# Optimization experiments

Measured on AMD Instinct MI355X. Metric: run time of the kernel, lower is better.

## Reference

```python
import jax, jax.numpy as jnp
import numpy as np
from jax import nn as jnn

N = 100000      # nodes
E = 3200000     # edges (avg degree 32)
G = 1024        # graphs in batch
F_IN = 3        # num_features (hard-coded in module)
D = 32          # dim (hard-coded in module)
BN_EPS = 1e-5


def setup_inputs() -> dict:
    key = jax.random.key(0)
    ks = jax.random.split(key, 24)
    def lin(k, i, o):
        return (jax.random.normal(k, (i, o), jnp.float32) / np.sqrt(i)).astype(jnp.float32)
    inp = {}
    inp["x"] = jax.random.normal(ks[0], (N, F_IN), jnp.float32)
    inp["edge_index"] = jax.random.randint(ks[1], (2, E), 0, N, dtype=jnp.int32)
    inp["batch"] = jnp.sort(jax.random.randint(ks[2], (N,), 0, G, dtype=jnp.int32))
    idx = 3
    in_dims = [F_IN, D, D]
    for l in (1, 2, 3):
        inp[f"W{l}a"] = lin(ks[idx], in_dims[l - 1], D); idx += 1
        inp[f"b{l}a"] = jnp.zeros((D,), jnp.float32)
        inp[f"W{l}b"] = lin(ks[idx], D, D); idx += 1
        inp[f"b{l}b"] = jnp.zeros((D,), jnp.float32)
        inp[f"g{l}"] = jnp.ones((D,), jnp.float32)            # BN gamma
        inp[f"be{l}"] = jnp.zeros((D,), jnp.float32)          # BN beta
        inp[f"m{l}"] = 0.1 * jax.random.normal(ks[idx], (D,), jnp.float32); idx += 1  # running mean
        inp[f"v{l}"] = jax.random.uniform(ks[idx], (D,), jnp.float32, 0.5, 1.5); idx += 1  # running var
    inp["Wf1"] = lin(ks[idx], D, D); idx += 1
    inp["bf1"] = jnp.zeros((D,), jnp.float32)
    inp["Wf2"] = lin(ks[idx], D, 1)
    inp["bf2"] = jnp.zeros((1,), jnp.float32)
    return inp


def reference(x, edge_index, batch,
              W1a, b1a, W1b, b1b, g1, be1, m1, v1,
              W2a, b2a, W2b, b2b, g2, be2, m2, v2,
              W3a, b3a, W3b, b3b, g3, be3, m3, v3,
              Wf1, bf1, Wf2, bf2):
    src, dst = edge_index[0], edge_index[1]

    def gin_bn(h, Wa, ba, Wb, bb, g, be, m, v):
        # GINConv (eps=0): nn(x + sum_{j->i} x_j); then relu; then BatchNorm1d (eval stats)
        agg = jax.ops.segment_sum(h[src], dst, num_segments=N) + h  # [N, d]
        h2 = jnn.relu(agg @ Wa + ba) @ Wb + bb                      # 2-layer MLP
        h2 = jnn.relu(h2)
        return g * (h2 - m) * jax.lax.rsqrt(v + BN_EPS) + be

    h = gin_bn(x, W1a, b1a, W1b, b1b, g1, be1, m1, v1)
    h = gin_bn(h, W2a, b2a, W2b, b2b, g2, be2, m2, v2)
    h = gin_bn(h, W3a, b3a, W3b, b3b, g3, be3, m3, v3)
    p = jax.ops.segment_sum(h, batch, num_segments=G)   # global_add_pool -> [G, D]
    p = jnn.relu(p @ Wf1 + bf1)
    # dropout p=0.5 is identity at inference
    return jnp.tanh(p @ Wf2 + bf2)                      # [G, 1]
```

## Files before the change

kernel.cpp:

```cpp
#include <hip/hip_runtime.h>
#include <math.h>

#define D 32
#define BN_EPS 1e-5f
#define NRANGE 512
#define RWC 196
#define MAXD 80
#define EPB 8192
#define K1_TPB 512
#define EPT (EPB / K1_TPB)

__global__ __launch_bounds__(K1_TPB) void build_part(
    const int* __restrict__ src, const int* __restrict__ dst,
    unsigned int* __restrict__ part, int* __restrict__ gcount,
    int E, int cap, int RW, unsigned long long M) {
    __shared__ unsigned int sorted[EPB];
    __shared__ unsigned short rid[EPB];
    __shared__ int cnt[NRANGE];
    __shared__ int exc[NRANGE];
    __shared__ int cur[NRANGE];
    __shared__ int gbase[NRANGE];
    int t = threadIdx.x;
    cnt[t] = 0;
    __syncthreads();

    int base = blockIdx.x * EPB;
    int n = min(EPB, E - base);

    unsigned int mypk[EPT];
    unsigned short myr[EPT];
#pragma unroll
    for (int k = 0; k < EPT; k++) {
        int i = t + k * K1_TPB;
        if (i < n) {
            int d = dst[base + i];
            int s = src[base + i];
            int r = (int)(((unsigned long long)d * M) >> 40);
            mypk[k] = ((unsigned)(d - r * RW) << 17) | (unsigned)s;
            myr[k] = (unsigned short)r;
            atomicAdd(&cnt[r], 1);
        } else myr[k] = 0xFFFFu;
    }
    __syncthreads();

    int inc = cnt[t];
    exc[t] = inc;
    __syncthreads();
    for (int s = 1; s < NRANGE; s <<= 1) {
        int u = (t >= s) ? exc[t - s] : 0;
        __syncthreads();
        exc[t] += u;
        __syncthreads();
    }
    int excl = exc[t] - cnt[t];
    __syncthreads();
    exc[t] = excl;
    cur[t] = excl;
    gbase[t] = atomicAdd(&gcount[t], cnt[t]);
    __syncthreads();

#pragma unroll
    for (int k = 0; k < EPT; k++) {
        if (myr[k] != 0xFFFFu) {
            int j = atomicAdd(&cur[myr[k]], 1);
            sorted[j] = mypk[k];
            rid[j] = myr[k];
        }
    }
    __syncthreads();

    for (int j = t; j < n; j += K1_TPB) {
        int r = rid[j];
        int pos = gbase[r] + (j - exc[r]);
        if (pos < cap) part[(size_t)r * cap + pos] = sorted[j];
    }
}

__global__ __launch_bounds__(1024) void build_csr(
    const unsigned int* __restrict__ part, const int* __restrict__ gcount,
    int* __restrict__ col, int* __restrict__ deg,
    const float* __restrict__ x, const float* __restrict__ W1a, float* __restrict__ y,
    int cap, int RW, int N, int maxd) {
    __shared__ int bucket[RWC * MAXD];
    __shared__ int rank_[RWC];
    int r = blockIdx.x, t = threadIdx.x, T = blockDim.x;
    for (int i = t; i < RW; i += T) rank_[i] = 0;
    __syncthreads();

    int count = gcount[r]; if (count > cap) count = cap;
    const unsigned int* p = part + (size_t)r * cap;
    int nbase = r * RW;
    for (int i = t; i < count; i += T) {
        unsigned int v = p[i];
        int dl = (int)(v >> 17);
        int slot = atomicAdd(&rank_[dl], 1);
        if (slot < maxd) bucket[dl * maxd + slot] = (int)(v & 0x1FFFFu);
    }
    __syncthreads();

    for (int i = t; i < RW; i += T) {
        int rk = rank_[i]; if (rk > maxd) rk = maxd;
        int pdg = (rk + 7) & ~7; if (pdg > maxd) pdg = maxd;
        int self = nbase + i;
        for (int k = rk; k < pdg; k++) bucket[i * maxd + k] = self;
    }
    __syncthreads();

    int nvalid = N - nbase; if (nvalid > RW) nvalid = RW;
    if (nvalid <= 0) return;
    int words = nvalid * maxd;
    int4* dst4 = (int4*)&col[(size_t)nbase * maxd];
    const int4* src4 = (const int4*)bucket;
    int nq = words >> 2;
    for (int i = t; i < nq; i += T) dst4[i] = src4[i];
    for (int i = t; i < nvalid; i += T) {
        int rk = rank_[i];
        deg[nbase + i] = rk < maxd ? rk : maxd;
    }

    int gidx = t >> 5, lane = t & 31;
    for (int nl = gidx; nl < nvalid; nl += 32) {
        int node = nbase + nl;
        float x0 = x[node * 3 + 0], x1 = x[node * 3 + 1], x2 = x[node * 3 + 2];
        float tv = x0 * W1a[0 * D + lane];
        tv = fmaf(x1, W1a[1 * D + lane], tv);
        tv = fmaf(x2, W1a[2 * D + lane], tv);
        y[(size_t)node * D + lane] = tv;
    }
}

__device__ __forceinline__ float gsum16(const float* __restrict__ hin, int creg, int off,
                                        int lane) {
    int i0 = __shfl(creg, off + 0, 32);
    int i1 = __shfl(creg, off + 1, 32);
    int i2 = __shfl(creg, off + 2, 32);
    int i3 = __shfl(creg, off + 3, 32);
    int i4 = __shfl(creg, off + 4, 32);
    int i5 = __shfl(creg, off + 5, 32);
    int i6 = __shfl(creg, off + 6, 32);
    int i7 = __shfl(creg, off + 7, 32);
    int i8 = __shfl(creg, off + 8, 32);
    int i9 = __shfl(creg, off + 9, 32);
    int i10 = __shfl(creg, off + 10, 32);
    int i11 = __shfl(creg, off + 11, 32);
    int i12 = __shfl(creg, off + 12, 32);
    int i13 = __shfl(creg, off + 13, 32);
    int i14 = __shfl(creg, off + 14, 32);
    int i15 = __shfl(creg, off + 15, 32);
    float a0 = hin[(size_t)i0 * D + lane];
    float a1 = hin[(size_t)i1 * D + lane];
    float a2 = hin[(size_t)i2 * D + lane];
    float a3 = hin[(size_t)i3 * D + lane];
    float a4 = hin[(size_t)i4 * D + lane];
    float a5 = hin[(size_t)i5 * D + lane];
    float a6 = hin[(size_t)i6 * D + lane];
    float a7 = hin[(size_t)i7 * D + lane];
    float a8 = hin[(size_t)i8 * D + lane];
    float a9 = hin[(size_t)i9 * D + lane];
    float a10 = hin[(size_t)i10 * D + lane];
    float a11 = hin[(size_t)i11 * D + lane];
    float a12 = hin[(size_t)i12 * D + lane];
    float a13 = hin[(size_t)i13 * D + lane];
    float a14 = hin[(size_t)i14 * D + lane];
    float a15 = hin[(size_t)i15 * D + lane];
    return ((((a0 + a1) + (a2 + a3)) + ((a4 + a5) + (a6 + a7))) +
            (((a8 + a9) + (a10 + a11)) + ((a12 + a13) + (a14 + a15))));
}

__device__ __forceinline__ float gsum8(const float* __restrict__ hin, int creg, int off,
                                       int lane) {
    int i0 = __shfl(creg, off + 0, 32);
    int i1 = __shfl(creg, off + 1, 32);
    int i2 = __shfl(creg, off + 2, 32);
    int i3 = __shfl(creg, off + 3, 32);
    int i4 = __shfl(creg, off + 4, 32);
    int i5 = __shfl(creg, off + 5, 32);
    int i6 = __shfl(creg, off + 6, 32);
    int i7 = __shfl(creg, off + 7, 32);
    float a0 = hin[(size_t)i0 * D + lane];
    float a1 = hin[(size_t)i1 * D + lane];
    float a2 = hin[(size_t)i2 * D + lane];
    float a3 = hin[(size_t)i3 * D + lane];
    float a4 = hin[(size_t)i4 * D + lane];
    float a5 = hin[(size_t)i5 * D + lane];
    float a6 = hin[(size_t)i6 * D + lane];
    float a7 = hin[(size_t)i7 * D + lane];
    return (((a0 + a1) + (a2 + a3)) + ((a4 + a5) + (a6 + a7)));
}

template <bool SKIP_WA, bool POOL>
__global__ void layer_fused(const float* __restrict__ hin, const int* __restrict__ deg,
                            const int* __restrict__ col, int maxd,
                            const float* __restrict__ Wa, const float* __restrict__ ba,
                            const float* __restrict__ Wb, const float* __restrict__ bb,
                            const float* __restrict__ g, const float* __restrict__ be,
                            const float* __restrict__ m, const float* __restrict__ v,
                            float* __restrict__ hout, const int* __restrict__ batch,
                            float* __restrict__ pool, int N) {
    long long gid = (long long)blockIdx.x * blockDim.x + threadIdx.x;
    int i = (int)(gid >> 5);
    int lane = (int)(gid & 31);
    bool valid = i < N;
    if (!POOL && !valid) return;

    float res = 0.f;
    int bg = -1;
    if (valid) {
        int dg = deg[i];
        if (dg > maxd) dg = maxd;
        int pdg = (dg + 7) & ~7; if (pdg > maxd) pdg = maxd;
        float acc = hin[(size_t)i * D + lane] * (float)(1 + dg - pdg);
        const int* cp = &col[(size_t)i * maxd];

        int cA = cp[lane];
        int cB = 0, cC = 0;
        if (pdg > 32) cB = cp[32 + lane];
        if (pdg > 64) cC = cp[64 + (lane & 15)];

        float s = 0.f;
        if (pdg >= 32) s += gsum16(hin, cA, 0, lane) + gsum16(hin, cA, 16, lane);
        if (pdg >= 64) s += gsum16(hin, cB, 0, lane) + gsum16(hin, cB, 16, lane);
        if (pdg & 16) {
            int st = pdg & ~31;
            int cr = st < 32 ? cA : (st < 64 ? cB : cC);
            s += gsum16(hin, cr, st & 31, lane);
        }
        if (pdg & 8) {
            int st = pdg & ~15;
            int cr = st < 32 ? cA : (st < 64 ? cB : cC);
            s += gsum8(hin, cr, st & 31, lane);
        }
        acc += s;

        float t;
        if (SKIP_WA) {
            t = fmaxf(acc + ba[lane], 0.f);
        } else {
            t = ba[lane];
#pragma unroll
            for (int k = 0; k < D; k++) {
                float ak = __shfl(acc, k, D);
                t = fmaf(ak, Wa[k * D + lane], t);
            }
            t = fmaxf(t, 0.f);
        }
        float o = bb[lane];
#pragma unroll
        for (int j = 0; j < D; j++) {
            float tj = __shfl(t, j, D);
            o = fmaf(tj, Wb[j * D + lane], o);
        }
        o = fmaxf(o, 0.f);
        res = g[lane] * (o - m[lane]) * rsqrtf(v[lane] + BN_EPS) + be[lane];
        if (POOL) bg = batch[i];
        else hout[(size_t)i * D + lane] = res;
    }

    if (POOL) {
        float other = __shfl_xor(res, 32, 64);
        int bo = __shfl_xor(bg, 32, 64);
        bool lowhalf = ((threadIdx.x & 32) == 0);
        if (bg >= 0) {
            if (bg == bo) {
                if (lowhalf) atomicAdd(&pool[(size_t)bg * D + lane], res + other);
            } else {
                atomicAdd(&pool[(size_t)bg * D + lane], res);
            }
        }
    }
}

__global__ void head_kernel(const float* __restrict__ pool, const float* __restrict__ Wf1,
                            const float* __restrict__ bf1, const float* __restrict__ Wf2,
                            const float* __restrict__ bf2, float* __restrict__ out, int G) {
    long long gid = (long long)blockIdx.x * blockDim.x + threadIdx.x;
    int gi = (int)(gid >> 5);
    int lane = (int)(gid & 31);
    if (gi >= G) return;
    float p = pool[(size_t)gi * D + lane];
    float q = bf1[lane];
#pragma unroll
    for (int j = 0; j < D; j++) {
        float pj = __shfl(p, j, D);
        q = fmaf(pj, Wf1[j * D + lane], q);
    }
    q = fmaxf(q, 0.f);
    float r = q * Wf2[lane];
#pragma unroll
    for (int off = 16; off; off >>= 1) r += __shfl_xor(r, off, D);
    if (lane == 0) out[gi] = tanhf(r + bf2[0]);
}

extern "C" void kernel_launch(void* const* d_in, const int* in_sizes, int n_in,
                              void* d_out, int out_size, void* d_ws, size_t ws_size,
                              hipStream_t stream) {
    const float* x = (const float*)d_in[0];
    const int* ei = (const int*)d_in[1];
    const int* batch = (const int*)d_in[2];
    const int E = in_sizes[1] / 2;
    const int N = in_sizes[2];
    const int G = out_size;
    const int* src = ei;
    const int* dst = ei + E;

    const float* P[3][8];
    for (int l = 0; l < 3; l++)
        for (int k = 0; k < 8; k++) P[l][k] = (const float*)d_in[3 + 8 * l + k];
    const float* Wf1 = (const float*)d_in[27];
    const float* bf1 = (const float*)d_in[28];
    const float* Wf2 = (const float*)d_in[29];
    const float* bf2 = (const float*)d_in[30];

    const int RW = (N + NRANGE - 1) / NRANGE;
    const unsigned long long M = ((1ull << 40) + RW - 1) / RW;
    int mean = (E + NRANGE - 1) / NRANGE;
    int cap = mean + mean / 8 + 64;
    cap = (cap + 7) & ~7;

    float* ws = (float*)d_ws;
    size_t off = 0;
    float* h0 = ws + off; off += (size_t)N * D;
    float* h1 = ws + off; off += (size_t)N * D;
    unsigned int* part = (unsigned int*)(ws + off); off += (size_t)NRANGE * cap;
    int* deg = (int*)(ws + off); off += N;
    int* gcount = (int*)(ws + off); off += NRANGE;
    float* pool = ws + off; off += (size_t)G * D;
    int* col = (int*)(ws + off);
    size_t remaining = ws_size / 4 > off ? ws_size / 4 - off : 0;
    int maxd = (int)(remaining / (size_t)N);
    if (maxd > MAXD) maxd = MAXD;
    maxd &= ~15;
    if (maxd < 16) maxd = 16;

    const int B = 256;
    long long tN32 = (long long)N * D;
    int nbp = (E + EPB - 1) / EPB;

    hipMemsetAsync(gcount, 0, (NRANGE + (size_t)G * D) * sizeof(int), stream);
    build_part<<<nbp, K1_TPB, 0, stream>>>(src, dst, part, gcount, E, cap, RW, M);
    build_csr<<<NRANGE, 1024, 0, stream>>>(part, gcount, col, deg, x, P[0][0], h0,
                                           cap, RW, N, maxd);

    layer_fused<true, false><<<(int)((tN32 + B - 1) / B), B, 0, stream>>>(
        h0, deg, col, maxd, P[0][0], P[0][1], P[0][2], P[0][3],
        P[0][4], P[0][5], P[0][6], P[0][7], h1, nullptr, nullptr, N);

    layer_fused<false, false><<<(int)((tN32 + B - 1) / B), B, 0, stream>>>(
        h1, deg, col, maxd, P[1][0], P[1][1], P[1][2], P[1][3],
        P[1][4], P[1][5], P[1][6], P[1][7], h0, nullptr, nullptr, N);

    layer_fused<false, true><<<(int)((tN32 + B - 1) / B), B, 0, stream>>>(
        h0, deg, col, maxd, P[2][0], P[2][1], P[2][2], P[2][3],
        P[2][4], P[2][5], P[2][6], P[2][7], h1, batch, pool, N);

    head_kernel<<<(int)(((long long)G * D + B - 1) / B), B, 0, stream>>>(
        pool, Wf1, bf1, Wf2, bf2, (float*)d_out, G);
}
```

Before: 336.2 us.

## Batch neighbor gathers in 32s, use nontemporal loads/stores, split FMA chains

Restructures the neighbor gather into 32-wide batches with tree reductions, so more independent loads are in flight per call. It also marks the degree, column and batch loads and the output stores as nontemporal to keep them from displacing the gathered features in cache. The two 32x32 matvecs now accumulate into four independent FMA chains to shorten dependency latency, and launch bounds of 256 are added. Costs are higher register pressure from the 32-element arrays, and the nontemporal store on hout may hurt the next layer, which rereads it.

```diff
diff --git a/kernel.cpp b/kernel.cpp
--- a/kernel.cpp
+++ b/kernel.cpp
@@ -129,74 +129,60 @@
     }
 }
 
+__device__ __forceinline__ float gsum32(const float* __restrict__ hin, int creg, int lane) {
+    float a[32];
+#pragma unroll
+    for (int k = 0; k < 32; k++) {
+        int idx = __shfl(creg, k, 32);
+        a[k] = hin[idx * D + lane];
+    }
+#pragma unroll
+    for (int st = 1; st < 32; st <<= 1)
+#pragma unroll
+        for (int k = 0; k < 32; k += (st << 1)) a[k] += a[k + st];
+    return a[0];
+}
+
 __device__ __forceinline__ float gsum16(const float* __restrict__ hin, int creg, int off,
                                         int lane) {
-    int i0 = __shfl(creg, off + 0, 32);
-    int i1 = __shfl(creg, off + 1, 32);
-    int i2 = __shfl(creg, off + 2, 32);
-    int i3 = __shfl(creg, off + 3, 32);
-    int i4 = __shfl(creg, off + 4, 32);
-    int i5 = __shfl(creg, off + 5, 32);
-    int i6 = __shfl(creg, off + 6, 32);
-    int i7 = __shfl(creg, off + 7, 32);
-    int i8 = __shfl(creg, off + 8, 32);
-    int i9 = __shfl(creg, off + 9, 32);
-    int i10 = __shfl(creg, off + 10, 32);
-    int i11 = __shfl(creg, off + 11, 32);
-    int i12 = __shfl(creg, off + 12, 32);
-    int i13 = __shfl(creg, off + 13, 32);
-    int i14 = __shfl(creg, off + 14, 32);
-    int i15 = __shfl(creg, off + 15, 32);
-    float a0 = hin[(size_t)i0 * D + lane];
-    float a1 = hin[(size_t)i1 * D + lane];
-    float a2 = hin[(size_t)i2 * D + lane];
-    float a3 = hin[(size_t)i3 * D + lane];
-    float a4 = hin[(size_t)i4 * D + lane];
-    float a5 = hin[(size_t)i5 * D + lane];
-    float a6 = hin[(size_t)i6 * D + lane];
-    float a7 = hin[(size_t)i7 * D + lane];
-    float a8 = hin[(size_t)i8 * D + lane];
-    float a9 = hin[(size_t)i9 * D + lane];
-    float a10 = hin[(size_t)i10 * D + lane];
-    float a11 = hin[(size_t)i11 * D + lane];
-    float a12 = hin[(size_t)i12 * D + lane];
-    float a13 = hin[(size_t)i13 * D + lane];
-    float a14 = hin[(size_t)i14 * D + lane];
-    float a15 = hin[(size_t)i15 * D + lane];
-    return ((((a0 + a1) + (a2 + a3)) + ((a4 + a5) + (a6 + a7))) +
-            (((a8 + a9) + (a10 + a11)) + ((a12 + a13) + (a14 + a15))));
+    float a[16];
+#pragma unroll
+    for (int k = 0; k < 16; k++) {
+        int idx = __shfl(creg, off + k, 32);
+        a[k] = hin[idx * D + lane];
+    }
+#pragma unroll
+    for (int st = 1; st < 16; st <<= 1)
+#pragma unroll
+        for (int k = 0; k < 16; k += (st << 1)) a[k] += a[k + st];
+    return a[0];
 }
 
 __device__ __forceinline__ float gsum8(const float* __restrict__ hin, int creg, int off,
                                        int lane) {
-    int i0 = __shfl(creg, off + 0, 32);
-    int i1 = __shfl(creg, off + 1, 32);
-    int i2 = __shfl(creg, off + 2, 32);
-    int i3 = __shfl(creg, off + 3, 32);
-    int i4 = __shfl(creg, off + 4, 32);
-    int i5 = __shfl(creg, off + 5, 32);
-    int i6 = __shfl(creg, off + 6, 32);
-    int i7 = __shfl(creg, off + 7, 32);
-    float a0 = hin[(size_t)i0 * D + lane];
-    float a1 = hin[(size_t)i1 * D + lane];
-    float a2 = hin[(size_t)i2 * D + lane];
-    float a3 = hin[(size_t)i3 * D + lane];
-    float a4 = hin[(size_t)i4 * D + lane];
-    float a5 = hin[(size_t)i5 * D + lane];
-    float a6 = hin[(size_t)i6 * D + lane];
-    float a7 = hin[(size_t)i7 * D + lane];
-    return (((a0 + a1) + (a2 + a3)) + ((a4 + a5) + (a6 + a7)));
+    float a[8];
+#pragma unroll
+    for (int k = 0; k < 8; k++) {
+        int idx = __shfl(creg, off + k, 32);
+        a[k] = hin[idx * D + lane];
+    }
+#pragma unroll
+    for (int st = 1; st < 8; st <<= 1)
+#pragma unroll
+        for (int k = 0; k < 8; k += (st << 1)) a[k] += a[k + st];
+    return a[0];
 }
 
 template <bool SKIP_WA, bool POOL>
-__global__ void layer_fused(const float* __restrict__ hin, const int* __restrict__ deg,
-                            const int* __restrict__ col, int maxd,
-                            const float* __restrict__ Wa, const float* __restrict__ ba,
-                            const float* __restrict__ Wb, const float* __restrict__ bb,
-                            const float* __restrict__ g, const float* __restrict__ be,
-                            const float* __restrict__ m, const float* __restrict__ v,
-                            float* __restrict__ hout, const int* __restrict__ batch,
-                            float* __restrict__ pool, int N) {
+__global__ __launch_bounds__(256) void layer_fused(
+    const float* __restrict__ hin, const int* __restrict__ deg,
+    const int* __restrict__ col, int maxd,
+    const float* __restrict__ Wa, const float* __restrict__ ba,
+    const float* __restrict__ Wb, const float* __restrict__ bb,
+    const float* __restrict__ g, const float* __restrict__ be,
+    const float* __restrict__ m, const float* __restrict__ v,
+    float* __restrict__ hout, const int* __restrict__ batch,
+    float* __restrict__ pool, int N) {
     long long gid = (long long)blockIdx.x * blockDim.x + threadIdx.x;
     int i = (int)(gid >> 5);
     int lane = (int)(gid & 31);
@@ -206,54 +192,52 @@
     float res = 0.f;
     int bg = -1;
     if (valid) {
-        int dg = deg[i];
+        int dg = __builtin_nontemporal_load(deg + i);
         if (dg > maxd) dg = maxd;
         int pdg = (dg + 7) & ~7; if (pdg > maxd) pdg = maxd;
         float acc = hin[(size_t)i * D + lane] * (float)(1 + dg - pdg);
         const int* cp = &col[(size_t)i * maxd];
 
-        int cA = cp[lane];
+        int cA = __builtin_nontemporal_load(cp + lane);
         int cB = 0, cC = 0;
-        if (pdg > 32) cB = cp[32 + lane];
-        if (pdg > 64) cC = cp[64 + (lane & 15)];
+        if (pdg > 32) cB = __builtin_nontemporal_load(cp + 32 + lane);
+        if (pdg > 64) cC = __builtin_nontemporal_load(cp + 64 + (lane & 15));
 
         float s = 0.f;
-        if (pdg >= 32) s += gsum16(hin, cA, 0, lane) + gsum16(hin, cA, 16, lane);
-        if (pdg >= 64) s += gsum16(hin, cB, 0, lane) + gsum16(hin, cB, 16, lane);
-        if (pdg & 16) {
-            int st = pdg & ~31;
-            int cr = st < 32 ? cA : (st < 64 ? cB : cC);
-            s += gsum16(hin, cr, st & 31, lane);
-        }
-        if (pdg & 8) {
-            int st = pdg & ~15;
-            int cr = st < 32 ? cA : (st < 64 ? cB : cC);
-            s += gsum8(hin, cr, st & 31, lane);
-        }
+        int rem = pdg;
+        if (rem >= 32) { s += gsum32(hin, cA, lane); rem -= 32; }
+        if (rem >= 32) { s += gsum32(hin, cB, lane); rem -= 32; }
+        int cR = (pdg < 32) ? cA : ((pdg < 64) ? cB : cC);
+        if (rem & 16) s += gsum16(hin, cR, 0, lane);
+        if (rem & 8)  s += gsum8(hin, cR, (rem & 16) ? 16 : 0, lane);
         acc += s;
 
         float t;
         if (SKIP_WA) {
             t = fmaxf(acc + ba[lane], 0.f);
         } else {
-            t = ba[lane];
-#pragma unroll
-            for (int k = 0; k < D; k++) {
-                float ak = __shfl(acc, k, D);
-                t = fmaf(ak, Wa[k * D + lane], t);
+            float t0 = ba[lane], t1 = 0.f, t2 = 0.f, t3 = 0.f;
+#pragma unroll
+            for (int k = 0; k < D; k += 4) {
+                t0 = fmaf(__shfl(acc, k + 0, D), Wa[(k + 0) * D + lane], t0);
+                t1 = fmaf(__shfl(acc, k + 1, D), Wa[(k + 1) * D + lane], t1);
+                t2 = fmaf(__shfl(acc, k + 2, D), Wa[(k + 2) * D + lane], t2);
+                t3 = fmaf(__shfl(acc, k + 3, D), Wa[(k + 3) * D + lane], t3);
             }
-            t = fmaxf(t, 0.f);
+            t = fmaxf((t0 + t1) + (t2 + t3), 0.f);
         }
-        float o = bb[lane];
-#pragma unroll
-        for (int j = 0; j < D; j++) {
-            float tj = __shfl(t, j, D);
-            o = fmaf(tj, Wb[j * D + lane], o);
+        float o0 = bb[lane], o1 = 0.f, o2 = 0.f, o3 = 0.f;
+#pragma unroll
+        for (int j = 0; j < D; j += 4) {
+            o0 = fmaf(__shfl(t, j + 0, D), Wb[(j + 0) * D + lane], o0);
+            o1 = fmaf(__shfl(t, j + 1, D), Wb[(j + 1) * D + lane], o1);
+            o2 = fmaf(__shfl(t, j + 2, D), Wb[(j + 2) * D + lane], o2);
+            o3 = fmaf(__shfl(t, j + 3, D), Wb[(j + 3) * D + lane], o3);
         }
-        o = fmaxf(o, 0.f);
+        float o = fmaxf((o0 + o1) + (o2 + o3), 0.f);
         res = g[lane] * (o - m[lane]) * rsqrtf(v[lane] + BN_EPS) + be[lane];
-        if (POOL) bg = batch[i];
-        else hout[(size_t)i * D + lane] = res;
+        if (POOL) bg = __builtin_nontemporal_load(batch + i);
+        else __builtin_nontemporal_store(res, &hout[(size_t)i * D + lane]);
     }
 
     if (POOL) {
```

Result: no change. 332.7 us (-1.0%).
